# Kernel tuning notes

Measured on AMD Instinct MI355X. Metric: run time of the kernel, lower is better.

## Reference

```python
import jax, jax.numpy as jnp
import numpy as np

B, NR, NT, NUM_ITER = 8192, 128, 64, 64


def setup_inputs() -> dict:
    key = jax.random.key(0)
    k1, k2, k3, k4 = jax.random.split(key, 4)
    Ht = jax.random.normal(k1, (B, NR, NT), dtype=jnp.float32) / np.sqrt(NR)
    yt = jax.random.normal(k2, (B, NR), dtype=jnp.float32)
    sigmat0 = jax.random.uniform(k3, (B,), dtype=jnp.float32) * 0.5 + 0.05
    # prior probabilities alpha[:,0] after slicing; keep strictly in (0,1)
    alpha = 0.2 + 0.6 * jax.random.uniform(k4, (NT,), dtype=jnp.float32)
    taui = jnp.ones((NUM_ITER,), dtype=jnp.float32)   # per-layer taui weights
    delta = jnp.full((NUM_ITER,), 0.1, dtype=jnp.float32)  # per-layer step sizes
    return {"yt": yt, "Ht": Ht, "sigmat0": sigmat0, "alpha": alpha,
            "taui": taui, "delta": delta}


def _cmd_step(s, c, HH, yH, sig2, taui_i, delta_i, t_x):
    # t_x is the temperature used inside tanh for xt (1.0 on the first layer,
    # |taui_i| otherwise); grad_x always uses |taui_i| as in the original code.
    taui_abs = jnp.abs(taui_i)
    xt = jnp.tanh((c + s) * 0.5 * t_x)                      # [B, NT]
    xHH = jnp.einsum('bn,bnm->bm', xt, HH)                  # [B, NT]
    grad_L = sig2 * jnp.tanh(s * 0.5) + 0.5 * taui_abs * (1.0 - xt ** 2) * (xHH - yH)
    return s - delta_i * grad_L


def reference(yt, Ht, sigmat0, alpha, taui, delta):
    # Precompute Gram matrix and matched filter output
    HH = jnp.einsum('brn,brm->bnm', Ht, Ht)                 # [B, NT, NT]
    yH = jnp.einsum('br,brn->bn', yt, Ht)                   # [B, NT]
    c = jnp.log(1.0 / alpha - 1.0)                          # [NT], prior offset
    sig2 = (sigmat0 ** 2)[:, None]                          # [B, 1]
    s0 = jnp.zeros_like(yH)                                 # [B, NT]

    # first layer: xt temperature fixed to 1 (first_iter=True)
    s = _cmd_step(s0, c, HH, yH, sig2, taui[0], delta[0], jnp.float32(1.0))

    def body(s, td):
        taui_i, delta_i = td
        s = _cmd_step(s, c, HH, yH, sig2, taui_i, delta_i, jnp.abs(taui_i))
        return s, None

    s, _ = jax.lax.scan(body, s, (taui[1:], delta[1:]))

    # final soft estimate uses the last layer's taui
    xt = jnp.tanh((c + s) * 0.5 * jnp.abs(taui[-1]))        # [B, NT]
    xt2 = xt[..., None]
    # m == [-1, 1] branch: ft = [P(m=-1), P(m=+1)]
    ft = jnp.concatenate([(1.0 - xt2) * 0.5, (1.0 + xt2) * 0.5], axis=-1)  # [B, NT, 2]
    return ft, xt
```

## Files before the change

### kernel.cpp

```cpp
#include <hip/hip_runtime.h>
#include <hip/hip_bf16.h>


typedef __attribute__((ext_vector_type(8))) short bf16x8;
typedef __attribute__((ext_vector_type(4))) float f32x4;
typedef __attribute__((ext_vector_type(2))) float f32x2;
typedef __attribute__((ext_vector_type(4))) int i32x4;

union FragCast { i32x4 i; bf16x8 h; };

#define NTc 64
#define NRc 128

__device__ __forceinline__ float tanh_fast(float x) {
  float u = __builtin_amdgcn_exp2f(x * 2.88539008177792681f);
  return 1.0f - 2.0f * __builtin_amdgcn_rcpf(u + 1.0f);
}

__device__ __forceinline__ f32x2 pkfma(f32x2 a, f32x2 b, f32x2 c) {
#if __has_builtin(__builtin_elementwise_fma)
  return __builtin_elementwise_fma(a, b, c);
#else
  return c + a * b;
#endif
}

__global__ __launch_bounds__(256, 3)
void cmdnet_bin_kernel(const float* __restrict__ yt, const float* __restrict__ Ht,
                       const float* __restrict__ sig0, const float* __restrict__ alpha,
                       const float* __restrict__ taui, const float* __restrict__ delta,
                       float* __restrict__ out, int B, int n_iter) {
  __shared__ __align__(16) float s_xt[4][64];

  const int tid = threadIdx.x;
  const int w = tid >> 6;
  const int l = tid & 63;
  const int g = l >> 4;
  const int c = l & 15;
  const int b = blockIdx.x * 4 + w;
  if (b >= B) return;

  const float* __restrict__ Hb = Ht + (size_t)b * (NRc * NTc);
  const float* __restrict__ yb = yt + (size_t)b * NRc;

  const bool hi2 = (g & 2) != 0;
  const bool odd = (g & 1) != 0;

  f32x4 acc[4][4];
  #pragma unroll
  for (int i = 0; i < 4; i++)
    #pragma unroll
    for (int j = 0; j < 4; j++) acc[i][j] = (f32x4)0.0f;

  float yhp[4] = {0.0f, 0.0f, 0.0f, 0.0f};

  const int base_l = (g * 8) * NTc + c;

  #pragma unroll
  for (int kk = 0; kk < 4; kk++) {
    const float4 ya  = *reinterpret_cast<const float4*>(yb + kk * 32 + g * 8);
    const float4 yb4 = *reinterpret_cast<const float4*>(yb + kk * 32 + g * 8 + 4);
    const float yv[8] = {ya.x, ya.y, ya.z, ya.w, yb4.x, yb4.y, yb4.z, yb4.w};

    FragCast fh[4], fl[4];
    #pragma unroll
    for (int p = 0; p < 4; p++) {
      #pragma unroll
      for (int jj = 0; jj < 4; jj++) {
        float v0 = Hb[base_l + kk * 32 * NTc + (2 * jj) * NTc + p * 16];
        float v1 = Hb[base_l + kk * 32 * NTc + (2 * jj + 1) * NTc + p * 16];
        yhp[p] = fmaf(yv[2 * jj], v0, yhp[p]);
        yhp[p] = fmaf(yv[2 * jj + 1], v1, yhp[p]);
        unsigned b0 = __float_as_uint(v0), b1 = __float_as_uint(v1);
        unsigned h0 = (b0 + 0x8000u) & 0xffff0000u;
        unsigned h1 = (b1 + 0x8000u) & 0xffff0000u;
        float r0 = v0 - __uint_as_float(h0);
        float r1 = v1 - __uint_as_float(h1);
        fh[p].i[jj] = (int)((h0 >> 16) | h1);
        fl[p].i[jj] = (int)(((__float_as_uint(r0) + 0x8000u) >> 16) |
                            ((__float_as_uint(r1) + 0x8000u) & 0xffff0000u));
      }
    }
    #pragma unroll
    for (int p = 0; p < 4; p++) {
      #pragma unroll
      for (int q = 0; q < 4; q++) {
        acc[p][q] = __builtin_amdgcn_mfma_f32_16x16x32_bf16(fh[p].h, fh[q].h, acc[p][q], 0, 0, 0);
        acc[p][q] = __builtin_amdgcn_mfma_f32_16x16x32_bf16(fh[p].h, fl[q].h, acc[p][q], 0, 0, 0);
        acc[p][q] = __builtin_amdgcn_mfma_f32_16x16x32_bf16(fl[p].h, fh[q].h, acc[p][q], 0, 0, 0);
      }
    }
  }

  float yH_l;
  {
    float sA = hi2 ? yhp[2] : yhp[0];
    float sB = hi2 ? yhp[3] : yhp[1];
    float oA = hi2 ? yhp[0] : yhp[2];
    float oB = hi2 ? yhp[1] : yhp[3];
    sA += __shfl_xor(oA, 32);
    sB += __shfl_xor(oB, 32);
    float keep = odd ? sB : sA;
    float send = odd ? sA : sB;
    yH_l = keep + __shfl_xor(send, 16);
  }

  const float a_l = alpha[l];
  const float c_l = logf(1.0f / a_l - 1.0f);
  const float sg = sig0[b];
  const float sig2 = sg * sg;

  float s = 0.0f;
  float taa = 1.0f;

  for (int it = 0; it < n_iter; it++) {
    const float de = delta[it];
    taa = fabsf(taui[it]);
    const float tx = (it == 0) ? 1.0f : taa;
    const float xtv = tanh_fast((c_l + s) * 0.5f * tx);

    s_xt[w][l] = xtv;

    f32x2 q0 = {0.0f, 0.0f}, q1 = {0.0f, 0.0f};
    f32x2 q2 = {0.0f, 0.0f}, q3 = {0.0f, 0.0f};
    #pragma unroll
    for (int i = 0; i < 4; i++) {
      const f32x4 xv = *reinterpret_cast<const f32x4*>(&s_xt[w][i * 16 + g * 4]);
      const f32x2 xlo = xv.xy, xhi = xv.zw;
      q0 = pkfma(xlo, acc[i][0].xy, q0); q0 = pkfma(xhi, acc[i][0].zw, q0);
      q1 = pkfma(xlo, acc[i][1].xy, q1); q1 = pkfma(xhi, acc[i][1].zw, q1);
      q2 = pkfma(xlo, acc[i][2].xy, q2); q2 = pkfma(xhi, acc[i][2].zw, q2);
      q3 = pkfma(xlo, acc[i][3].xy, q3); q3 = pkfma(xhi, acc[i][3].zw, q3);
    }
    float p0 = q0.x + q0.y, p1 = q1.x + q1.y;
    float p2 = q2.x + q2.y, p3 = q3.x + q3.y;

    float sA = hi2 ? p2 : p0;
    float sB = hi2 ? p3 : p1;
    float oA = hi2 ? p0 : p2;
    float oB = hi2 ? p1 : p3;
    sA += __shfl_xor(oA, 32);
    sB += __shfl_xor(oB, 32);
    float keep = odd ? sB : sA;
    float send = odd ? sA : sB;
    const float xHH = keep + __shfl_xor(send, 16);

    const float grad = sig2 * tanh_fast(s * 0.5f) +
                       0.5f * taa * (1.0f - xtv * xtv) * (xHH - yH_l);
    s = s - de * grad;
  }

  const float xtf = tanh_fast((c_l + s) * 0.5f * taa);
  float2 ft;
  ft.x = 0.5f * (1.0f - xtf);
  ft.y = 0.5f * (1.0f + xtf);
  *reinterpret_cast<float2*>(out + ((size_t)b * NTc + l) * 2) = ft;
  out[(size_t)B * NTc * 2 + (size_t)b * NTc + l] = xtf;
}

extern "C" void kernel_launch(void* const* d_in, const int* in_sizes, int n_in,
                              void* d_out, int out_size, void* d_ws, size_t ws_size,
                              hipStream_t stream) {
  const float* yt    = (const float*)d_in[0];
  const float* Ht    = (const float*)d_in[1];
  const float* sig0  = (const float*)d_in[2];
  const float* alpha = (const float*)d_in[3];
  const float* taui  = (const float*)d_in[4];
  const float* delta = (const float*)d_in[5];
  const int B = in_sizes[2];
  const int n_iter = in_sizes[4];

  const int blocks = (B + 3) / 4;
  hipLaunchKernelGGL(cmdnet_bin_kernel, dim3(blocks), dim3(256), 0, stream,
                     yt, Ht, sig0, alpha, taui, delta, (float*)d_out, B, n_iter);
}
```

Before: 414.3 us.

## Use parallel xor shuffles, readlane params, hoisted prior grad, higher occupancy

Replaces the serial two-stage shuffle reduction with a single stage of three independent cross-lane exchanges (one ds_swizzle, two shfl_xor), which shortens the dependency chain inside each iteration. Per-layer taui and delta are loaded once into lanes and broadcast with readlane, so the loop no longer issues scalar memory loads. The sigma-prior tanh term is computed right after s is updated, taking it off the critical path of the next iteration. Launch bounds are raised to four blocks per CU, which may constrain registers given the 64 accumulator floats per lane. Readlane also assumes n_iter is at most 64.

```diff
diff --git a/kernel.cpp b/kernel.cpp
--- a/kernel.cpp
+++ b/kernel.cpp
@@ -25,7 +25,28 @@
 #endif
 }
 
-__global__ __launch_bounds__(256, 3)
+__device__ __forceinline__ float rdlane(float v, int lane) {
+  return __int_as_float(__builtin_amdgcn_readlane(__float_as_int(v), lane));
+}
+
+__device__ __forceinline__ float swz_xor16(float x) {
+  return __int_as_float(__builtin_amdgcn_ds_swizzle(__float_as_int(x), 0x401F));
+}
+
+__device__ __forceinline__ float reduce_scatter4p(float p0, float p1,
+                                                  float p2, float p3, int g) {
+  const bool b0 = (g & 1) != 0, b1 = (g & 2) != 0;
+  const float own = b1 ? (b0 ? p3 : p2) : (b0 ? p1 : p0);
+  const float r1  = b0 ? (b1 ? p2 : p0) : (b1 ? p3 : p1);
+  const float r2  = b1 ? (b0 ? p1 : p0) : (b0 ? p3 : p2);
+  const float r3  = b1 ? (b0 ? p0 : p1) : (b0 ? p2 : p3);
+  const float u1 = swz_xor16(r1);
+  const float u2 = __shfl_xor(r2, 32);
+  const float u3 = __shfl_xor(r3, 48);
+  return (own + u1) + (u2 + u3);
+}
+
+__global__ __launch_bounds__(256, 4)
 void cmdnet_bin_kernel(const float* __restrict__ yt, const float* __restrict__ Ht,
                        const float* __restrict__ sig0, const float* __restrict__ alpha,
                        const float* __restrict__ taui, const float* __restrict__ delta,
@@ -42,9 +63,6 @@
 
   const float* __restrict__ Hb = Ht + (size_t)b * (NRc * NTc);
   const float* __restrict__ yb = yt + (size_t)b * NRc;
-
-  const bool hi2 = (g & 2) != 0;
-  const bool odd = (g & 1) != 0;
 
   f32x4 acc[4][4];
   #pragma unroll
@@ -92,32 +110,27 @@
     }
   }
 
-  float yH_l;
-  {
-    float sA = hi2 ? yhp[2] : yhp[0];
-    float sB = hi2 ? yhp[3] : yhp[1];
-    float oA = hi2 ? yhp[0] : yhp[2];
-    float oB = hi2 ? yhp[1] : yhp[3];
-    sA += __shfl_xor(oA, 32);
-    sB += __shfl_xor(oB, 32);
-    float keep = odd ? sB : sA;
-    float send = odd ? sA : sB;
-    yH_l = keep + __shfl_xor(send, 16);
-  }
+  const float yH_l = reduce_scatter4p(yhp[0], yhp[1], yhp[2], yhp[3], g);
 
   const float a_l = alpha[l];
   const float c_l = logf(1.0f / a_l - 1.0f);
   const float sg = sig0[b];
   const float sig2 = sg * sg;
 
+  const int li = (l < n_iter) ? l : 0;
+  const float v_ta = taui[li];
+  const float v_de = delta[li];
+
   float s = 0.0f;
+  float gp = 0.0f;
   float taa = 1.0f;
 
   for (int it = 0; it < n_iter; it++) {
-    const float de = delta[it];
-    taa = fabsf(taui[it]);
-    const float tx = (it == 0) ? 1.0f : taa;
-    const float xtv = tanh_fast((c_l + s) * 0.5f * tx);
+    const float ta = rdlane(v_ta, it);
+    const float de = rdlane(v_de, it);
+    taa = fabsf(ta);
+    const float th = (it == 0) ? 0.5f : 0.5f * taa;
+    const float xtv = tanh_fast((c_l + s) * th);
 
     s_xt[w][l] = xtv;
 
@@ -132,22 +145,11 @@
       q2 = pkfma(xlo, acc[i][2].xy, q2); q2 = pkfma(xhi, acc[i][2].zw, q2);
       q3 = pkfma(xlo, acc[i][3].xy, q3); q3 = pkfma(xhi, acc[i][3].zw, q3);
     }
-    float p0 = q0.x + q0.y, p1 = q1.x + q1.y;
-    float p2 = q2.x + q2.y, p3 = q3.x + q3.y;
+    const float xHH = reduce_scatter4p(q0.x + q0.y, q1.x + q1.y,
+                                       q2.x + q2.y, q3.x + q3.y, g);
 
-    float sA = hi2 ? p2 : p0;
-    float sB = hi2 ? p3 : p1;
-    float oA = hi2 ? p0 : p2;
-    float oB = hi2 ? p1 : p3;
-    sA += __shfl_xor(oA, 32);
-    sB += __shfl_xor(oB, 32);
-    float keep = odd ? sB : sA;
-    float send = odd ? sA : sB;
-    const float xHH = keep + __shfl_xor(send, 16);
-
-    const float grad = sig2 * tanh_fast(s * 0.5f) +
-                       0.5f * taa * (1.0f - xtv * xtv) * (xHH - yH_l);
-    s = s - de * grad;
+    s = s - de * (gp + 0.5f * taa * (1.0f - xtv * xtv) * (xHH - yH_l));
+    gp = sig2 * tanh_fast(s * 0.5f);
   }
 
   const float xtf = tanh_fast((c_l + s) * 0.5f * taa);
```

After: 414.4 us. About the same (+0.0%).
